# Optimization experiments

Measured on AMD Instinct MI355X. Metric: run time of the kernel, lower is better.

Reference implementation:

```python
import jax, jax.numpy as jnp
import numpy as np
from jax import lax

BATCH, SEQ_LEN, INPUT_DIM, OUTPUT_DIM = 64, 1000, 512, 512
KERNEL_WIDTH = 5  # context [-2, 2] with full_context=True -> range(-2, 3)


def setup_inputs() -> dict:
    key = jax.random.key(0)
    k1, k2, k3 = jax.random.split(key, 3)
    stdv = 1.0 / np.sqrt(INPUT_DIM)
    x = jax.random.normal(k1, (BATCH, SEQ_LEN, INPUT_DIM), dtype=jnp.float32)
    kernel = stdv * jax.random.normal(k2, (OUTPUT_DIM, INPUT_DIM, KERNEL_WIDTH), dtype=jnp.float32)
    bias = stdv * jax.random.normal(k3, (OUTPUT_DIM,), dtype=jnp.float32)
    return {"x": x, "kernel": kernel, "bias": bias}


def reference(x, kernel, bias):
    # x: [B, T, C_in] -> [B, C_in, T]
    xt = jnp.transpose(x, (0, 2, 1))
    # Contiguous full context == single VALID conv over time.
    # Original loop: for each valid step i, gather x[:, :, context+i] and conv1d,
    # which for context=range(-2,3) is exactly this strided convolution.
    out = lax.conv_general_dilated(
        xt, kernel,
        window_strides=(1,), padding="VALID",
        dimension_numbers=("NCH", "OIH", "NCH"),
    )  # [B, C_out, T - K + 1]
    out = out + bias[None, :, None]
    # ReLU then transpose back to [B, T_valid, C_out]
    return jnp.transpose(jax.nn.relu(out), (0, 2, 1))
```

## Files before the change

kernel.cpp:

```cpp
#include <hip/hip_runtime.h>
#include <hip/hip_bf16.h>


#define BATCH 64
#define SEQ   1000
#define CIN   512
#define COUT  512
#define KW    5
#define TOUT  996
#define KTOT  2560
#define MTOT  63744
#define MT    498
#define NT    4

typedef __bf16 bf16x8 __attribute__((ext_vector_type(8)));
typedef float  f32x4  __attribute__((ext_vector_type(4)));

__device__ __forceinline__ void gload_lds16(const void* g, void* l) {
  __builtin_amdgcn_global_load_lds(
      (const __attribute__((address_space(1))) void*)g,
      (__attribute__((address_space(3))) void*)l,
      16, 0, 0);
}

__global__ void cvt_x_kernel(const float* __restrict__ x, __bf16* __restrict__ xb, int n) {
  int i = (blockIdx.x * blockDim.x + threadIdx.x) * 8;
  if (i >= n) return;
  float4 f0 = *(const float4*)(x + i);
  float4 f1 = *(const float4*)(x + i + 4);
  bf16x8 v;
  v[0] = (__bf16)f0.x; v[1] = (__bf16)f0.y; v[2] = (__bf16)f0.z; v[3] = (__bf16)f0.w;
  v[4] = (__bf16)f1.x; v[5] = (__bf16)f1.y; v[6] = (__bf16)f1.z; v[7] = (__bf16)f1.w;
  *(bf16x8*)(xb + i) = v;
}

__global__ void cvt_w_kernel(const float* __restrict__ k, __bf16* __restrict__ wt) {
  int idx = blockIdx.x * blockDim.x + threadIdx.x;
  if (idx >= COUT * KTOT) return;
  int o  = idx / KTOT;
  int r  = idx - o * KTOT;
  int kw = r >> 9;
  int c  = r & 511;
  wt[idx] = (__bf16)k[(o * CIN + c) * KW + kw];
}

__global__ __launch_bounds__(256)
void tdnn_gemm_kernel(const __bf16* __restrict__ Xb, const __bf16* __restrict__ Wt,
                      const float* __restrict__ bias, float* __restrict__ out) {
  __shared__ __align__(16) __bf16 Alds[128 * 32];
  __shared__ __align__(16) __bf16 Blds[128 * 32];

  const int tid  = threadIdx.x;
  const int wave = tid >> 6;
  const int lane = tid & 63;

  int bid = blockIdx.x;
  int swz = (bid & 7) * (MT * NT / 8) + (bid >> 3);
  const int bm = swz >> 2;
  const int bn = swz & 3;
  const int m0 = bm * 128;
  const int n0 = bn * 128;

  const int rA0 = (wave * 2 + 0) * 16 + (lane >> 2);
  const int rA1 = (wave * 2 + 1) * 16 + (lane >> 2);
  const int kof = (lane & 3) * 8;

  int mA0 = m0 + rA0, mA1 = m0 + rA1;
  int b0 = mA0 / TOUT, t0 = mA0 - b0 * TOUT;
  int b1 = mA1 / TOUT, t1 = mA1 - b1 * TOUT;
  const __bf16* gA0 = Xb + ((size_t)(b0 * SEQ + t0) * CIN) + kof;
  const __bf16* gA1 = Xb + ((size_t)(b1 * SEQ + t1) * CIN) + kof;
  const __bf16* gB0 = Wt + (size_t)(n0 + rA0) * KTOT + kof;
  const __bf16* gB1 = Wt + (size_t)(n0 + rA1) * KTOT + kof;

  char* ldsA0 = (char*)Alds + (wave * 2 + 0) * 1024;
  char* ldsA1 = (char*)Alds + (wave * 2 + 1) * 1024;
  char* ldsB0 = (char*)Blds + (wave * 2 + 0) * 1024;
  char* ldsB1 = (char*)Blds + (wave * 2 + 1) * 1024;

  const int wr = wave >> 1;
  const int wc = wave & 1;

  f32x4 acc[4][4];
  const f32x4 z = {0.f, 0.f, 0.f, 0.f};
#pragma unroll
  for (int i = 0; i < 4; i++)
#pragma unroll
    for (int j = 0; j < 4; j++) acc[i][j] = z;

  const int frow = lane & 15;
  const int fk   = (lane >> 4) * 8;

  for (int kk = 0; kk < KTOT; kk += 32) {
    gload_lds16(gA0 + kk, ldsA0);
    gload_lds16(gA1 + kk, ldsA1);
    gload_lds16(gB0 + kk, ldsB0);
    gload_lds16(gB1 + kk, ldsB1);
    __syncthreads();

    bf16x8 a[4], b[4];
#pragma unroll
    for (int i = 0; i < 4; i++)
      a[i] = *(const bf16x8*)&Alds[(wr * 64 + i * 16 + frow) * 32 + fk];
#pragma unroll
    for (int i = 0; i < 4; i++)
      b[i] = *(const bf16x8*)&Blds[(wc * 64 + i * 16 + frow) * 32 + fk];

#pragma unroll
    for (int i = 0; i < 4; i++)
#pragma unroll
      for (int j = 0; j < 4; j++)
        acc[i][j] = __builtin_amdgcn_mfma_f32_16x16x32_bf16(a[i], b[j], acc[i][j], 0, 0, 0);

    __syncthreads();
  }

  const int ccol = lane & 15;
  const int crow = (lane >> 4) * 4;
  float bv[4];
#pragma unroll
  for (int nj = 0; nj < 4; nj++)
    bv[nj] = bias[n0 + wc * 64 + nj * 16 + ccol];

#pragma unroll
  for (int mi = 0; mi < 4; mi++) {
    const int mrow = m0 + wr * 64 + mi * 16 + crow;
#pragma unroll
    for (int nj = 0; nj < 4; nj++) {
      const int ocol = n0 + wc * 64 + nj * 16 + ccol;
#pragma unroll
      for (int j = 0; j < 4; j++) {
        float v = acc[mi][nj][j] + bv[nj];
        v = v > 0.f ? v : 0.f;
        out[(size_t)(mrow + j) * COUT + ocol] = v;
      }
    }
  }
}

extern "C" void kernel_launch(void* const* d_in, const int* in_sizes, int n_in,
                              void* d_out, int out_size, void* d_ws, size_t ws_size,
                              hipStream_t stream) {
  const float* x      = (const float*)d_in[0];
  const float* kernel = (const float*)d_in[1];
  const float* bias   = (const float*)d_in[2];
  float* out          = (float*)d_out;

  __bf16* xb = (__bf16*)d_ws;
  __bf16* wt = (__bf16*)((char*)d_ws + (size_t)BATCH * SEQ * CIN * 2);

  const int nx = BATCH * SEQ * CIN;
  cvt_x_kernel<<<nx / 8 / 256, 256, 0, stream>>>(x, xb, nx);
  cvt_w_kernel<<<(COUT * KTOT + 255) / 256, 256, 0, stream>>>(kernel, wt);
  tdnn_gemm_kernel<<<MT * NT, 256, 0, stream>>>(xb, wt, bias, out);
}
```

Before: 236.4 us.

## Rewrite GEMM as 256x256 tile, double-buffered LDS pipeline with XOR swizzle

Replaces the 128x128 single-buffered GEMM with 256x256 tiles, 512-thread workgroups and a 64-wide K step. Operands are double-buffered in XOR-swizzled LDS and staged in quarters that are interleaved with MFMA phases under explicit waitcnt, barriers and setprio. The XCD-aware block swizzle is also reworked. The aim is to hide global-load latency, cut LDS bank conflicts and raise arithmetic intensity per load, at the cost of more registers (32 accumulators per wave) and more barriers per iteration.

```diff
diff --git a/kernel.cpp b/kernel.cpp
--- a/kernel.cpp
+++ b/kernel.cpp
@@ -6,12 +6,13 @@
 #define SEQ   1000
 #define CIN   512
 #define COUT  512
-#define KW    5
 #define TOUT  996
 #define KTOT  2560
 #define MTOT  63744
-#define MT    498
-#define NT    4
+#define NKT   40
+#define MT    249
+#define NT    2
+#define NWG   (MT*NT)
 
 typedef __bf16 bf16x8 __attribute__((ext_vector_type(8)));
 typedef float  f32x4  __attribute__((ext_vector_type(4)));
@@ -19,9 +20,14 @@
 __device__ __forceinline__ void gload_lds16(const void* g, void* l) {
   __builtin_amdgcn_global_load_lds(
       (const __attribute__((address_space(1))) void*)g,
-      (__attribute__((address_space(3))) void*)l,
-      16, 0, 0);
-}
+      (__attribute__((address_space(3))) void*)l, 16, 0, 0);
+}
+
+#define BAR()   __builtin_amdgcn_s_barrier()
+#define LGKM0() asm volatile("s_waitcnt lgkmcnt(0)" ::: "memory")
+#define VM4()   asm volatile("s_waitcnt vmcnt(4)" ::: "memory")
+#define VM0()   asm volatile("s_waitcnt vmcnt(0)" ::: "memory")
+#define PRIO(x) __builtin_amdgcn_s_setprio(x)
 
 __global__ void cvt_x_kernel(const float* __restrict__ x, __bf16* __restrict__ xb, int n) {
   int i = (blockIdx.x * blockDim.x + threadIdx.x) * 8;
@@ -41,95 +47,164 @@
   int r  = idx - o * KTOT;
   int kw = r >> 9;
   int c  = r & 511;
-  wt[idx] = (__bf16)k[(o * CIN + c) * KW + kw];
-}
-
-__global__ __launch_bounds__(256)
+  wt[idx] = (__bf16)k[(o * CIN + c) * 5 + kw];
+}
+
+#define STAGE_A(buf, h, kt) do { \
+    char* d_ = (char*)&Ab[buf][h][0][0]; \
+    gload_lds16(Xb + offA##h##0 + (kt)*64, d_ + dof0); \
+    gload_lds16(Xb + offA##h##1 + (kt)*64, d_ + dof1); } while (0)
+#define STAGE_B(buf, h, kt) do { \
+    char* d_ = (char*)&Bb[buf][h][0][0]; \
+    gload_lds16(Wt + offB##h##0 + (kt)*64, d_ + dof0); \
+    gload_lds16(Wt + offB##h##1 + (kt)*64, d_ + dof1); } while (0)
+
+#define RD_A(mi, ks) (*(const bf16x8*)(Abase + ((mi)*16 + frow)*128 + ((((ks)*64 + fkb)) ^ xorv)))
+#define RD_B(nj, ks) (*(const bf16x8*)(Bbase + (brow0 + (nj)*16 + frow)*128 + ((((ks)*64 + fkb)) ^ xorv)))
+
+__global__ __launch_bounds__(512, 2)
 void tdnn_gemm_kernel(const __bf16* __restrict__ Xb, const __bf16* __restrict__ Wt,
                       const float* __restrict__ bias, float* __restrict__ out) {
-  __shared__ __align__(16) __bf16 Alds[128 * 32];
-  __shared__ __align__(16) __bf16 Blds[128 * 32];
+  __shared__ __bf16 Ab[2][2][128][64];
+  __shared__ __bf16 Bb[2][2][128][64];
 
   const int tid  = threadIdx.x;
   const int wave = tid >> 6;
   const int lane = tid & 63;
+  const int wr = wave >> 2;
+  const int wc = wave & 3;
 
   int bid = blockIdx.x;
-  int swz = (bid & 7) * (MT * NT / 8) + (bid >> 3);
-  const int bm = swz >> 2;
-  const int bn = swz & 3;
-  const int m0 = bm * 128;
-  const int n0 = bn * 128;
-
-  const int rA0 = (wave * 2 + 0) * 16 + (lane >> 2);
-  const int rA1 = (wave * 2 + 1) * 16 + (lane >> 2);
-  const int kof = (lane & 3) * 8;
-
-  int mA0 = m0 + rA0, mA1 = m0 + rA1;
-  int b0 = mA0 / TOUT, t0 = mA0 - b0 * TOUT;
-  int b1 = mA1 / TOUT, t1 = mA1 - b1 * TOUT;
-  const __bf16* gA0 = Xb + ((size_t)(b0 * SEQ + t0) * CIN) + kof;
-  const __bf16* gA1 = Xb + ((size_t)(b1 * SEQ + t1) * CIN) + kof;
-  const __bf16* gB0 = Wt + (size_t)(n0 + rA0) * KTOT + kof;
-  const __bf16* gB1 = Wt + (size_t)(n0 + rA1) * KTOT + kof;
-
-  char* ldsA0 = (char*)Alds + (wave * 2 + 0) * 1024;
-  char* ldsA1 = (char*)Alds + (wave * 2 + 1) * 1024;
-  char* ldsB0 = (char*)Blds + (wave * 2 + 0) * 1024;
-  char* ldsB1 = (char*)Blds + (wave * 2 + 1) * 1024;
-
-  const int wr = wave >> 1;
-  const int wc = wave & 1;
-
-  f32x4 acc[4][4];
+  int xcd = bid & 7, jj = bid >> 3;
+  const int q = NWG >> 3, r = NWG & 7;
+  int swz = (xcd < r ? xcd * (q + 1) : r * (q + 1) + (xcd - r) * q) + jj;
+  const int m0 = (swz >> 1) * 256;
+  const int n0 = (swz & 1) * 256;
+
+  int offA00, offA01, offA10, offA11, offB00, offB01, offB10, offB11, dof0, dof1;
+  {
+    int o16, row, ce, m, b, tt;
+#define MKOFF(l, A0, A1, B0, B1, D) \
+    o16 = (l)*512 + tid; row = o16 >> 3; \
+    ce  = ((((o16 & 7) << 4) ^ ((row & 7) << 4)) >> 1); \
+    D   = o16 * 16; \
+    m = m0 + 0*128 + row; b = m / TOUT; tt = m - b * TOUT; \
+    A0 = (b * SEQ + tt) * CIN + ce; \
+    m = m0 + 1*128 + row; b = m / TOUT; tt = m - b * TOUT; \
+    A1 = (b * SEQ + tt) * CIN + ce; \
+    B0 = (n0 + 0*128 + row) * KTOT + ce; \
+    B1 = (n0 + 1*128 + row) * KTOT + ce;
+    MKOFF(0, offA00, offA10, offB00, offB10, dof0)
+    MKOFF(1, offA01, offA11, offB01, offB11, dof1)
+#undef MKOFF
+  }
+
+  const int frow = lane & 15;
+  const int fkb  = (lane >> 4) << 4;
+  const int xorv = (frow & 7) << 4;
+  const int brow0 = (wc & 1) * 64;
+
+  f32x4 acc[8][4];
   const f32x4 z = {0.f, 0.f, 0.f, 0.f};
 #pragma unroll
-  for (int i = 0; i < 4; i++)
+  for (int i = 0; i < 8; i++)
 #pragma unroll
     for (int j = 0; j < 4; j++) acc[i][j] = z;
 
-  const int frow = lane & 15;
-  const int fk   = (lane >> 4) * 8;
-
-  for (int kk = 0; kk < KTOT; kk += 32) {
-    gload_lds16(gA0 + kk, ldsA0);
-    gload_lds16(gA1 + kk, ldsA1);
-    gload_lds16(gB0 + kk, ldsB0);
-    gload_lds16(gB1 + kk, ldsB1);
-    __syncthreads();
-
-    bf16x8 a[4], b[4];
-#pragma unroll
-    for (int i = 0; i < 4; i++)
-      a[i] = *(const bf16x8*)&Alds[(wr * 64 + i * 16 + frow) * 32 + fk];
-#pragma unroll
-    for (int i = 0; i < 4; i++)
-      b[i] = *(const bf16x8*)&Blds[(wc * 64 + i * 16 + frow) * 32 + fk];
-
-#pragma unroll
-    for (int i = 0; i < 4; i++)
-#pragma unroll
-      for (int j = 0; j < 4; j++)
-        acc[i][j] = __builtin_amdgcn_mfma_f32_16x16x32_bf16(a[i], b[j], acc[i][j], 0, 0, 0);
-
-    __syncthreads();
+  STAGE_A(0, 0, 0); STAGE_A(0, 1, 0);
+  STAGE_B(0, 0, 0); STAGE_B(0, 1, 0);
+  STAGE_A(1, 0, 1); STAGE_A(1, 1, 1);
+  VM4();
+  BAR();
+
+  for (int t = 0; t < NKT; ++t) {
+    const int c  = t & 1;
+    const int oo = c ^ 1;
+    const bool s1 = (t + 1 < NKT);
+    const bool s2 = (t + 2 < NKT);
+
+    const char* Abase = (const char*)&Ab[c][wr][0][0];
+    const char* Bbase = (const char*)&Bb[c][wc >> 1][0][0];
+
+    bf16x8 a[8][2], b[4][2];
+
+#pragma unroll
+    for (int mi = 0; mi < 4; ++mi) { a[mi][0] = RD_A(mi, 0); a[mi][1] = RD_A(mi, 1); }
+#pragma unroll
+    for (int nj = 0; nj < 2; ++nj) { b[nj][0] = RD_B(nj, 0); b[nj][1] = RD_B(nj, 1); }
+    if (s1) STAGE_B(oo, 0, t + 1);
+    BAR(); LGKM0();
+    PRIO(1);
+#pragma unroll
+    for (int mi = 0; mi < 4; ++mi)
+#pragma unroll
+      for (int nj = 0; nj < 2; ++nj) {
+        acc[mi][nj] = __builtin_amdgcn_mfma_f32_16x16x32_bf16(a[mi][0], b[nj][0], acc[mi][nj], 0, 0, 0);
+        acc[mi][nj] = __builtin_amdgcn_mfma_f32_16x16x32_bf16(a[mi][1], b[nj][1], acc[mi][nj], 0, 0, 0);
+      }
+    PRIO(0);
+    BAR();
+
+#pragma unroll
+    for (int mi = 4; mi < 8; ++mi) { a[mi][0] = RD_A(mi, 0); a[mi][1] = RD_A(mi, 1); }
+#pragma unroll
+    for (int nj = 2; nj < 4; ++nj) { b[nj][0] = RD_B(nj, 0); b[nj][1] = RD_B(nj, 1); }
+    if (s1) STAGE_B(oo, 1, t + 1);
+    BAR(); LGKM0();
+    PRIO(1);
+#pragma unroll
+    for (int mi = 4; mi < 8; ++mi)
+#pragma unroll
+      for (int nj = 0; nj < 2; ++nj) {
+        acc[mi][nj] = __builtin_amdgcn_mfma_f32_16x16x32_bf16(a[mi][0], b[nj][0], acc[mi][nj], 0, 0, 0);
+        acc[mi][nj] = __builtin_amdgcn_mfma_f32_16x16x32_bf16(a[mi][1], b[nj][1], acc[mi][nj], 0, 0, 0);
+      }
+    PRIO(0);
+    BAR();
+
+    if (s2) STAGE_A(c, 0, t + 2);
+    BAR();
+    PRIO(1);
+#pragma unroll
+    for (int mi = 0; mi < 4; ++mi)
+#pragma unroll
+      for (int nj = 2; nj < 4; ++nj) {
+        acc[mi][nj] = __builtin_amdgcn_mfma_f32_16x16x32_bf16(a[mi][0], b[nj][0], acc[mi][nj], 0, 0, 0);
+        acc[mi][nj] = __builtin_amdgcn_mfma_f32_16x16x32_bf16(a[mi][1], b[nj][1], acc[mi][nj], 0, 0, 0);
+      }
+    PRIO(0);
+    BAR();
+
+    if (s2) STAGE_A(c, 1, t + 2);
+    if (s2) { VM4(); } else { VM0(); }
+    BAR();
+    PRIO(1);
+#pragma unroll
+    for (int mi = 4; mi < 8; ++mi)
+#pragma unroll
+      for (int nj = 2; nj < 4; ++nj) {
+        acc[mi][nj] = __builtin_amdgcn_mfma_f32_16x16x32_bf16(a[mi][0], b[nj][0], acc[mi][nj], 0, 0, 0);
+        acc[mi][nj] = __builtin_amdgcn_mfma_f32_16x16x32_bf16(a[mi][1], b[nj][1], acc[mi][nj], 0, 0, 0);
+      }
+    PRIO(0);
+    BAR();
   }
 
   const int ccol = lane & 15;
   const int crow = (lane >> 4) * 4;
   float bv[4];
 #pragma unroll
-  for (int nj = 0; nj < 4; nj++)
+  for (int nj = 0; nj < 4; ++nj)
     bv[nj] = bias[n0 + wc * 64 + nj * 16 + ccol];
 
 #pragma unroll
-  for (int mi = 0; mi < 4; mi++) {
-    const int mrow = m0 + wr * 64 + mi * 16 + crow;
-#pragma unroll
-    for (int nj = 0; nj < 4; nj++) {
+  for (int mi = 0; mi < 8; ++mi) {
+    const int mrow = m0 + wr * 128 + mi * 16 + crow;
+#pragma unroll
+    for (int nj = 0; nj < 4; ++nj) {
       const int ocol = n0 + wc * 64 + nj * 16 + ccol;
 #pragma unroll
-      for (int j = 0; j < 4; j++) {
+      for (int j = 0; j < 4; ++j) {
         float v = acc[mi][nj][j] + bv[nj];
         v = v > 0.f ? v : 0.f;
         out[(size_t)(mrow + j) * COUT + ocol] = v;
@@ -152,5 +227,5 @@
   const int nx = BATCH * SEQ * CIN;
   cvt_x_kernel<<<nx / 8 / 256, 256, 0, stream>>>(x, xb, nx);
   cvt_w_kernel<<<(COUT * KTOT + 255) / 256, 256, 0, stream>>>(kernel, wt);
-  tdnn_gemm_kernel<<<MT * NT, 256, 0, stream>>>(xb, wt, bias, out);
-}
+  tdnn_gemm_kernel<<<NWG, 512, 0, stream>>>(xb, wt, bias, out);
+}
```

Measured after the change: 193.7 us. 18.1% less time.

## Restructure GEMM into 256x256 tiles with a 4-stage LDS pipeline and register-resident weights

Applied to the files above, without the earlier changes.

Enlarges the output tile to 256x256 with 512-thread workgroups and a K step of 64. The A operand is loaded into a 4-buffer, XOR-swizzled LDS ring filled by direct global-to-LDS loads two stages ahead. Weights are pre-permuted into MFMA fragment order so each wave loads them straight into registers, double-buffered. Explicit vmcnt waits, single barriers, setprio and XCD-aware block remapping replace the two syncthreads per iteration. This removes the serialised load-then-compute pattern and raises data reuse per tile, at the cost of higher register and LDS pressure and fewer workgroups.

```diff
diff --git a/kernel.cpp b/kernel.cpp
--- a/kernel.cpp
+++ b/kernel.cpp
@@ -6,12 +6,13 @@
 #define SEQ   1000
 #define CIN   512
 #define COUT  512
-#define KW    5
 #define TOUT  996
 #define KTOT  2560
 #define MTOT  63744
-#define MT    498
-#define NT    4
+#define NKT   40
+#define MT    249
+#define NT    2
+#define NWG   (MT*NT)
 
 typedef __bf16 bf16x8 __attribute__((ext_vector_type(8)));
 typedef float  f32x4  __attribute__((ext_vector_type(4)));
@@ -19,9 +20,16 @@
 __device__ __forceinline__ void gload_lds16(const void* g, void* l) {
   __builtin_amdgcn_global_load_lds(
       (const __attribute__((address_space(1))) void*)g,
-      (__attribute__((address_space(3))) void*)l,
-      16, 0, 0);
-}
+      (__attribute__((address_space(3))) void*)l, 16, 0, 0);
+}
+
+#define BAR()    __builtin_amdgcn_s_barrier()
+#define VM12()   asm volatile("s_waitcnt vmcnt(12)" ::: "memory")
+#define VM8()    asm volatile("s_waitcnt vmcnt(8)"  ::: "memory")
+#define VM4()    asm volatile("s_waitcnt vmcnt(4)"  ::: "memory")
+#define PRIO(x)  __builtin_amdgcn_s_setprio(x)
+#define SCHED0() __builtin_amdgcn_sched_barrier(0)
+#define MFMA(d, x, y) d = __builtin_amdgcn_mfma_f32_16x16x32_bf16(x, y, d, 0, 0, 0)
 
 __global__ void cvt_x_kernel(const float* __restrict__ x, __bf16* __restrict__ xb, int n) {
   int i = (blockIdx.x * blockDim.x + threadIdx.x) * 8;
@@ -36,100 +44,150 @@
 
 __global__ void cvt_w_kernel(const float* __restrict__ k, __bf16* __restrict__ wt) {
   int idx = blockIdx.x * blockDim.x + threadIdx.x;
-  if (idx >= COUT * KTOT) return;
-  int o  = idx / KTOT;
-  int r  = idx - o * KTOT;
-  int kw = r >> 9;
-  int c  = r & 511;
-  wt[idx] = (__bf16)k[(o * CIN + c) * KW + kw];
-}
-
-__global__ __launch_bounds__(256)
-void tdnn_gemm_kernel(const __bf16* __restrict__ Xb, const __bf16* __restrict__ Wt,
+  if (idx >= 80 * 32 * 512) return;
+  int j  = idx & 7;
+  int l  = (idx >> 3) & 63;
+  int t1 = idx >> 9;
+  int ob = t1 & 31;
+  int ks = t1 >> 5;
+  int o  = ob * 16 + (l & 15);
+  int kk = ks * 32 + ((l >> 4) & 3) * 8 + j;
+  int c  = kk & 511, kw = kk >> 9;
+  wt[idx] = (__bf16)k[(o * CIN + c) * 5 + kw];
+}
+
+#define STAGE(buf, kt) do { \
+    char* d_ = (char*)Ab + ((buf) << 15); \
+    gload_lds16(Xb + offA0 + (kt) * 64, d_ + dof0); \
+    gload_lds16(Xb + offA1 + (kt) * 64, d_ + dof1); \
+    gload_lds16(Xb + offA2 + (kt) * 64, d_ + dof2); \
+    gload_lds16(Xb + offA3 + (kt) * 64, d_ + dof3); } while (0)
+
+#define LOADB(bn, Tn) do { \
+    const char* p_ = Wglob + (size_t)(Tn) * 65536; \
+    bn[0][0] = *(const bf16x8*)(p_ +     0); bn[0][1] = *(const bf16x8*)(p_ + 32768); \
+    bn[1][0] = *(const bf16x8*)(p_ +  1024); bn[1][1] = *(const bf16x8*)(p_ + 33792); \
+    bn[2][0] = *(const bf16x8*)(p_ +  2048); bn[2][1] = *(const bf16x8*)(p_ + 34816); \
+    bn[3][0] = *(const bf16x8*)(p_ +  3072); bn[3][1] = *(const bf16x8*)(p_ + 35840); } while (0)
+
+#define TILE(T, bc, bn) do { \
+    const bool s1_ = (T) + 1 < NKT, s2_ = (T) + 2 < NKT; \
+    if (s1_) LOADB(bn, (T) + 1); \
+    if (s2_) STAGE(((T) + 2) & 3, (T) + 2); \
+    const char* Ac_ = Aw + (((T) & 3) << 15); \
+    bf16x8 a_[4][2]; \
+    _Pragma("unroll") \
+    for (int mi = 0; mi < 4; ++mi) { \
+      a_[mi][0] = *(const bf16x8*)(Ac_ + mi * 2048 + off0); \
+      a_[mi][1] = *(const bf16x8*)(Ac_ + mi * 2048 + off1); \
+    } \
+    PRIO(1); \
+    _Pragma("unroll") \
+    for (int mi = 0; mi < 4; ++mi) \
+      _Pragma("unroll") \
+      for (int nj = 0; nj < 4; ++nj) { \
+        MFMA(acc[mi][nj], a_[mi][0], bc[nj][0]); \
+        MFMA(acc[mi][nj], a_[mi][1], bc[nj][1]); \
+      } \
+    PRIO(0); \
+    _Pragma("unroll") \
+    for (int mi = 0; mi < 4; ++mi) { \
+      a_[mi][0] = *(const bf16x8*)(Ac_ + (mi + 4) * 2048 + off0); \
+      a_[mi][1] = *(const bf16x8*)(Ac_ + (mi + 4) * 2048 + off1); \
+    } \
+    PRIO(1); \
+    _Pragma("unroll") \
+    for (int mi = 0; mi < 4; ++mi) \
+      _Pragma("unroll") \
+      for (int nj = 0; nj < 4; ++nj) { \
+        MFMA(acc[mi + 4][nj], a_[mi][0], bc[nj][0]); \
+        MFMA(acc[mi + 4][nj], a_[mi][1], bc[nj][1]); \
+      } \
+    PRIO(0); \
+    SCHED0(); \
+    if (s2_) { VM12(); } else if (s1_) { VM8(); } \
+    if (s1_) BAR(); \
+  } while (0)
+
+__global__ __launch_bounds__(512, 2)
+void tdnn_gemm_kernel(const __bf16* __restrict__ Xb, const __bf16* __restrict__ Wt2,
                       const float* __restrict__ bias, float* __restrict__ out) {
-  __shared__ __align__(16) __bf16 Alds[128 * 32];
-  __shared__ __align__(16) __bf16 Blds[128 * 32];
+  __shared__ __bf16 Ab[4][256][64];
 
   const int tid  = threadIdx.x;
   const int wave = tid >> 6;
   const int lane = tid & 63;
+  const int wr = wave >> 2;
+  const int wc = wave & 3;
 
   int bid = blockIdx.x;
-  int swz = (bid & 7) * (MT * NT / 8) + (bid >> 3);
-  const int bm = swz >> 2;
-  const int bn = swz & 3;
-  const int m0 = bm * 128;
-  const int n0 = bn * 128;
-
-  const int rA0 = (wave * 2 + 0) * 16 + (lane >> 2);
-  const int rA1 = (wave * 2 + 1) * 16 + (lane >> 2);
-  const int kof = (lane & 3) * 8;
-
-  int mA0 = m0 + rA0, mA1 = m0 + rA1;
-  int b0 = mA0 / TOUT, t0 = mA0 - b0 * TOUT;
-  int b1 = mA1 / TOUT, t1 = mA1 - b1 * TOUT;
-  const __bf16* gA0 = Xb + ((size_t)(b0 * SEQ + t0) * CIN) + kof;
-  const __bf16* gA1 = Xb + ((size_t)(b1 * SEQ + t1) * CIN) + kof;
-  const __bf16* gB0 = Wt + (size_t)(n0 + rA0) * KTOT + kof;
-  const __bf16* gB1 = Wt + (size_t)(n0 + rA1) * KTOT + kof;
-
-  char* ldsA0 = (char*)Alds + (wave * 2 + 0) * 1024;
-  char* ldsA1 = (char*)Alds + (wave * 2 + 1) * 1024;
-  char* ldsB0 = (char*)Blds + (wave * 2 + 0) * 1024;
-  char* ldsB1 = (char*)Blds + (wave * 2 + 1) * 1024;
-
-  const int wr = wave >> 1;
-  const int wc = wave & 1;
-
-  f32x4 acc[4][4];
+  int xcd = bid & 7, jj = bid >> 3;
+  const int q = NWG >> 3, r = NWG & 7;
+  int swz = (xcd < r ? xcd * (q + 1) : r * (q + 1) + (xcd - r) * q) + jj;
+  const int m0 = (swz >> 1) * 256;
+  const int n0 = (swz & 1) * 256;
+
+  int offA0, offA1, offA2, offA3, dof0, dof1, dof2, dof3;
+  {
+    int o16, row, ce, m, b, tt;
+#define MKOFF(l, A, D) \
+    o16 = (l) * 512 + tid; row = o16 >> 3; \
+    ce  = ((((o16 & 7) << 4) ^ ((row & 7) << 4)) >> 1); \
+    D   = o16 * 16; \
+    m = m0 + row; b = m / TOUT; tt = m - b * TOUT; \
+    A = (b * SEQ + tt) * CIN + ce;
+    MKOFF(0, offA0, dof0)
+    MKOFF(1, offA1, dof1)
+    MKOFF(2, offA2, dof2)
+    MKOFF(3, offA3, dof3)
+#undef MKOFF
+  }
+
+  const int frow = lane & 15;
+  const int fkb  = (lane >> 4) << 4;
+  const int xorv = (frow & 7) << 4;
+  const int off0 = fkb ^ xorv;
+  const int off1 = (64 + fkb) ^ xorv;
+  const char* Aw = (const char*)Ab + (wr * 128 + frow) * 128;
+
+  const int obW = (n0 >> 4) + wc * 4;
+  const char* Wglob = (const char*)Wt2 + obW * 1024 + lane * 16;
+
+  f32x4 acc[8][4];
   const f32x4 z = {0.f, 0.f, 0.f, 0.f};
 #pragma unroll
-  for (int i = 0; i < 4; i++)
+  for (int i = 0; i < 8; i++)
 #pragma unroll
     for (int j = 0; j < 4; j++) acc[i][j] = z;
 
-  const int frow = lane & 15;
-  const int fk   = (lane >> 4) * 8;
-
-  for (int kk = 0; kk < KTOT; kk += 32) {
-    gload_lds16(gA0 + kk, ldsA0);
-    gload_lds16(gA1 + kk, ldsA1);
-    gload_lds16(gB0 + kk, ldsB0);
-    gload_lds16(gB1 + kk, ldsB1);
-    __syncthreads();
-
-    bf16x8 a[4], b[4];
-#pragma unroll
-    for (int i = 0; i < 4; i++)
-      a[i] = *(const bf16x8*)&Alds[(wr * 64 + i * 16 + frow) * 32 + fk];
-#pragma unroll
-    for (int i = 0; i < 4; i++)
-      b[i] = *(const bf16x8*)&Blds[(wc * 64 + i * 16 + frow) * 32 + fk];
-
-#pragma unroll
-    for (int i = 0; i < 4; i++)
-#pragma unroll
-      for (int j = 0; j < 4; j++)
-        acc[i][j] = __builtin_amdgcn_mfma_f32_16x16x32_bf16(a[i], b[j], acc[i][j], 0, 0, 0);
-
-    __syncthreads();
+  bf16x8 bA[4][2], bB[4][2];
+
+  LOADB(bA, 0);
+  STAGE(0, 0);
+  STAGE(1, 1);
+  VM4();
+  BAR();
+
+  for (int T = 0; T < NKT; T += 2) {
+    TILE(T,     bA, bB);
+    TILE(T + 1, bB, bA);
   }
 
   const int ccol = lane & 15;
   const int crow = (lane >> 4) * 4;
   float bv[4];
 #pragma unroll
-  for (int nj = 0; nj < 4; nj++)
+  for (int nj = 0; nj < 4; ++nj)
     bv[nj] = bias[n0 + wc * 64 + nj * 16 + ccol];
 
 #pragma unroll
-  for (int mi = 0; mi < 4; mi++) {
-    const int mrow = m0 + wr * 64 + mi * 16 + crow;
-#pragma unroll
-    for (int nj = 0; nj < 4; nj++) {
+  for (int mi = 0; mi < 8; ++mi) {
+    const int mrow = m0 + wr * 128 + mi * 16 + crow;
+#pragma unroll
+    for (int nj = 0; nj < 4; ++nj) {
       const int ocol = n0 + wc * 64 + nj * 16 + ccol;
 #pragma unroll
-      for (int j = 0; j < 4; j++) {
+      for (int j = 0; j < 4; ++j) {
         float v = acc[mi][nj][j] + bv[nj];
         v = v > 0.f ? v : 0.f;
         out[(size_t)(mrow + j) * COUT + ocol] = v;
@@ -146,11 +204,11 @@
   const float* bias   = (const float*)d_in[2];
   float* out          = (float*)d_out;
 
-  __bf16* xb = (__bf16*)d_ws;
-  __bf16* wt = (__bf16*)((char*)d_ws + (size_t)BATCH * SEQ * CIN * 2);
+  __bf16* xb  = (__bf16*)d_ws;
+  __bf16* wt2 = (__bf16*)((char*)d_ws + (size_t)BATCH * SEQ * CIN * 2);
 
   const int nx = BATCH * SEQ * CIN;
   cvt_x_kernel<<<nx / 8 / 256, 256, 0, stream>>>(x, xb, nx);
-  cvt_w_kernel<<<(COUT * KTOT + 255) / 256, 256, 0, stream>>>(kernel, wt);
-  tdnn_gemm_kernel<<<MT * NT, 256, 0, stream>>>(xb, wt, bias, out);
-}
+  cvt_w_kernel<<<(80 * 32 * 512 + 255) / 256, 256, 0, stream>>>(kernel, wt2);
+  tdnn_gemm_kernel<<<NWG, 512, 0, stream>>>(xb, wt2, bias, out);
+}
```

Result: faster. 201.1 us (-14.9%).
